# Kernel optimization log

Hardware: AMD Instinct MI355X
Metric: run time of the kernel (lower is better)

## Reference

```python
import jax, jax.numpy as jnp
import numpy as np

B, T, H = 4, 2048, 1024
N, D = 16, 64  # heads, key_dim (= value_dim)
SCALE = 1.0 / float(D) ** 0.5


def setup_inputs() -> dict:
    key = jax.random.key(0)
    ks = jax.random.split(key, 10)
    s = 0.02
    return {
        "query": jax.random.normal(ks[0], (B, T, H), jnp.float32),
        "value": jax.random.normal(ks[1], (B, T, H), jnp.float32),
        "Wq": jax.random.normal(ks[2], (N * D, H), jnp.float32) * s,
        "bq": jnp.zeros((N * D,), jnp.float32),
        "Wk": jax.random.normal(ks[3], (N * D, H), jnp.float32) * s,
        "bk": jnp.zeros((N * D,), jnp.float32),
        "Wv": jax.random.normal(ks[4], (N * D, H), jnp.float32) * s,
        "bv": jnp.zeros((N * D,), jnp.float32),
        "Wo": jax.random.normal(ks[5], (H, N * D), jnp.float32) * s,
        "bo": jnp.zeros((H,), jnp.float32),
    }


def reference(query, value, Wq, bq, Wk, bk, Wv, bv, Wo, bo):
    key_in = value  # key=None path: key = value
    q = (query @ Wq.T + bq).reshape(B, -1, N, D)   # [B,T,N,D]
    k = (key_in @ Wk.T + bk).reshape(B, -1, N, D)  # [B,S,N,D]
    v = (value @ Wv.T + bv).reshape(B, -1, N, D)   # [B,S,N,D]
    # scores [T,S,B,N], softmax over S (axis=1), scaled dot-product
    scores = jnp.einsum('btnd,bsnd->tsbn', q, k) * SCALE
    attn = jax.nn.softmax(scores, axis=1)
    # output [B,T,N,D]
    out = jnp.einsum('tsbn,bsnd->btnd', attn, v)
    out = out.reshape(B, T, N * D)
    return out @ Wo.T + bo
```

## Files before the change

### kernel.cpp

```cpp
#include <hip/hip_runtime.h>
#include <cstdint>
#include <cstddef>

typedef unsigned short u16;
typedef __bf16 bf16x8 __attribute__((ext_vector_type(8)));
typedef __bf16 bf16x2 __attribute__((ext_vector_type(2)));
typedef float f32x4 __attribute__((ext_vector_type(4)));
typedef float f32x16 __attribute__((ext_vector_type(16)));

#define B_   4
#define T_   2048
#define H_   1024
#define NH_  16
#define DH_  64
#define M_   (B_ * T_)
#define KDIM 1024
#define QSCALE 0.18033688011112042f

#define BM 128
#define BN 128
#define BK 32

__device__ __forceinline__ u16 f2bf(float f) {
    unsigned u = __float_as_uint(f);
    unsigned r = (u + 0x7fffu + ((u >> 16) & 1u)) >> 16;
    return (u16)r;
}

__device__ __forceinline__ unsigned packbf2(float a, float b) {
    bf16x2 v = { (__bf16)a, (__bf16)b };
    return __builtin_bit_cast(unsigned, v);
}

__device__ __forceinline__ float exp2_fast(float x) {
#if __has_builtin(__builtin_amdgcn_exp2f)
    return __builtin_amdgcn_exp2f(x);
#else
    return exp2f(x);
#endif
}

__device__ __forceinline__ void plswap(unsigned &a, unsigned &b) {
#if __has_builtin(__builtin_amdgcn_permlane32_swap)
    auto r = __builtin_amdgcn_permlane32_swap(a, b, false, false);
    a = (unsigned)r[0]; b = (unsigned)r[1];
#else
    int hi = (threadIdx.x & 32);
    unsigned x = (unsigned)__shfl_xor((int)(hi ? b : a), 32);
    unsigned na = hi ? x : a;
    unsigned nb = hi ? b : x;
    a = na; b = nb;
#endif
}

__device__ __forceinline__ void gload16(const void* g, void* l) {
    __builtin_amdgcn_global_load_lds(
        (const __attribute__((address_space(1))) unsigned int*)g,
        (__attribute__((address_space(3))) unsigned int*)l,
        16, 0, 0);
}

__device__ __forceinline__ f32x16 mfma32(bf16x8 a, bf16x8 b, f32x16 c) {
    return __builtin_amdgcn_mfma_f32_32x32x16_bf16(a, b, c, 0, 0, 0);
}

__global__ __launch_bounds__(256) void f2bf_hex(
    const float* s0, u16* d0, int n0, const float* s1, u16* d1, int n1,
    const float* s2, u16* d2, int n2, const float* s3, u16* d3, int n3,
    const float* s4, u16* d4, int n4j, const float* s5, u16* d5, int n5)
{
    const float* s; u16* d; int n;
    switch (blockIdx.y) {
        case 0: s = s0; d = d0; n = n0; break;
        case 1: s = s1; d = d1; n = n1; break;
        case 2: s = s2; d = d2; n = n2; break;
        case 3: s = s3; d = d3; n = n3; break;
        case 4: s = s4; d = d4; n = n4j; break;
        default: s = s5; d = d5; n = n5; break;
    }
    int i = blockIdx.x * blockDim.x + threadIdx.x;
    int stride = gridDim.x * blockDim.x;
    for (; i < n; i += stride) {
        float4 f = reinterpret_cast<const float4*>(s)[i];
        ushort4 o;
        o.x = f2bf(f.x); o.y = f2bf(f.y); o.z = f2bf(f.z); o.w = f2bf(f.w);
        reinterpret_cast<ushort4*>(d)[i] = o;
    }
}

__device__ __forceinline__ void gemm_core(
    const u16* __restrict__ X, const u16* __restrict__ W,
    const float* __restrict__ bias,
    u16* __restrict__ dst_bf, float* __restrict__ dst_f,
    float scale, int mode, int r0, int c0)
{
    __shared__ u16 lds[17408];
    char* ldsA = (char*)lds;
    char* ldsB = (char*)lds + 8192;

    const int tid = threadIdx.x;
    const int wid = tid >> 6;
    const int l15 = tid & 15;
    const int l4  = (tid & 63) >> 4;
    const int wr = wid >> 1, wc = wid & 1;

    const u16* gA = X + (size_t)(r0 + (tid >> 2)) * KDIM + (tid & 3) * 8;
    const u16* gB = W + (size_t)(c0 + (tid >> 2)) * KDIM + (tid & 3) * 8;
    char* sA0 = ldsA + wid * 1024;
    char* sA1 = ldsA + 4096 + wid * 1024;
    char* sB0 = ldsB + wid * 1024;
    char* sB1 = ldsB + 4096 + wid * 1024;

    f32x4 acc[4][4];
#pragma unroll
    for (int m = 0; m < 4; ++m)
#pragma unroll
        for (int n = 0; n < 4; ++n) acc[m][n] = (f32x4){0.f, 0.f, 0.f, 0.f};

    gload16(gA, sA0); gload16(gA + 64 * KDIM, sA1);
    gload16(gB, sB0); gload16(gB + 64 * KDIM, sB1);

    const int arow = wr * 64 + l15;
    const int brow = wc * 64 + l15;

    for (int kt = 0; kt < KDIM / BK; ++kt) {
        __syncthreads();
        bf16x8 a[4], b[4];
#pragma unroll
        for (int m = 0; m < 4; ++m)
            a[m] = *(const bf16x8*)(ldsA + (arow + m * 16) * 64 + l4 * 16);
#pragma unroll
        for (int n = 0; n < 4; ++n)
            b[n] = *(const bf16x8*)(ldsB + (brow + n * 16) * 64 + l4 * 16);
#pragma unroll
        for (int m = 0; m < 4; ++m)
#pragma unroll
            for (int n = 0; n < 4; ++n)
                acc[m][n] = __builtin_amdgcn_mfma_f32_16x16x32_bf16(a[m], b[n], acc[m][n], 0, 0, 0);
        __syncthreads();
        if (kt + 1 < KDIM / BK) {
            const u16* pa = gA + (kt + 1) * BK;
            const u16* pb = gB + (kt + 1) * BK;
            gload16(pa, sA0); gload16(pa + 64 * KDIM, sA1);
            gload16(pb, sB0); gload16(pb + 64 * KDIM, sB1);
        }
    }

    if (mode == 2) {
#pragma unroll
        for (int m = 0; m < 4; ++m)
#pragma unroll
            for (int n = 0; n < 4; ++n) {
                int cg = c0 + wc * 64 + n * 16 + l15;
                float bv = bias[cg];
                int rg = r0 + wr * 64 + m * 16 + l4 * 4;
#pragma unroll
                for (int j = 0; j < 4; ++j)
                    dst_f[(size_t)(rg + j) * H_ + cg] = acc[m][n][j] + bv;
            }
    } else if (mode == 0) {
#pragma unroll
        for (int m = 0; m < 4; ++m)
#pragma unroll
            for (int n = 0; n < 4; ++n) {
                int cg = c0 + wc * 64 + n * 16 + l15;
                int head = cg >> 6, d = cg & 63;
                float bv = bias[cg];
                int rg = r0 + wr * 64 + m * 16 + l4 * 4;
#pragma unroll
                for (int j = 0; j < 4; ++j) {
                    int r = rg + j;
                    int b = r >> 11, t = r & (T_ - 1);
                    dst_bf[(((size_t)(b * NH_ + head) * T_ + t) << 6) + d] =
                        f2bf((acc[m][n][j] + bv) * scale);
                }
            }
    } else {
        __syncthreads();
        u16 (*ldsT)[136] = (u16(*)[136])lds;
#pragma unroll
        for (int m = 0; m < 4; ++m)
#pragma unroll
            for (int n = 0; n < 4; ++n) {
                int cl = wc * 64 + n * 16 + l15;
                float bv = bias[c0 + cl];
                int rl = wr * 64 + m * 16 + l4 * 4;
#pragma unroll
                for (int j = 0; j < 4; ++j)
                    ldsT[cl][rl + j] = f2bf(acc[m][n][j] + bv);
            }
        __syncthreads();
        int b = r0 >> 11, tb = r0 & (T_ - 1);
#pragma unroll
        for (int it = 0; it < 8; ++it) {
            int chunk = tid + it * 256;
            int cl = chunk >> 4;
            int r8 = (chunk & 15) << 3;
            int cg = c0 + cl;
            int head = cg >> 6, d = cg & 63;
            uint4 v = *(const uint4*)&ldsT[cl][r8];
            *(uint4*)&dst_bf[((size_t)((b * NH_ + head) * DH_ + d) * T_) + tb + r8] = v;
        }
    }
}

__global__ __launch_bounds__(256) void gemm_qkv(
    const u16* __restrict__ qbf, const u16* __restrict__ vbf,
    const u16* __restrict__ Wqb, const u16* __restrict__ Wkb, const u16* __restrict__ Wvb,
    const float* __restrict__ bq, const float* __restrict__ bk, const float* __restrict__ bv,
    u16* __restrict__ Qd, u16* __restrict__ Kd, u16* __restrict__ Vtd)
{
    const int orig = blockIdx.y * 24 + blockIdx.x;
    const int swz = (orig & 7) * 192 + (orig >> 3);
    const int bx = swz % 24;
    const int by = swz / 24;
    const int seg = bx >> 3;
    const int r0 = by * BM;
    const int c0 = (bx & 7) * BN;

    if (seg == 0)
        gemm_core(qbf, Wqb, bq, Qd, nullptr, QSCALE, 0, r0, c0);
    else if (seg == 1)
        gemm_core(vbf, Wkb, bk, Kd, nullptr, 1.0f, 0, r0, c0);
    else
        gemm_core(vbf, Wvb, bv, Vtd, nullptr, 1.0f, 1, r0, c0);
}

__global__ __launch_bounds__(256) void gemm_out(
    const u16* __restrict__ AO, const u16* __restrict__ Wob,
    const float* __restrict__ bo, float* __restrict__ out)
{
    const int orig = blockIdx.y * 8 + blockIdx.x;
    const int swz = (orig & 7) * 64 + (orig >> 3);
    const int bx = swz & 7;
    const int by = swz >> 3;
    gemm_core(AO, Wob, bo, nullptr, out, 1.0f, 2, by * BM, bx * BN);
}

#define KVB 64

__global__ __launch_bounds__(256) void attn32(
    const u16* __restrict__ Q, const u16* __restrict__ K,
    const u16* __restrict__ Vt, u16* __restrict__ AO)
{
    __shared__ u16 lds[16384];
    char* const base = (char*)lds;

    const int tid = threadIdx.x;
    const int wid = tid >> 6;
    const int lane = tid & 63;
    const int l31 = lane & 31;
    const int hi = lane >> 5;

    const int orig = blockIdx.y * 16 + blockIdx.x;
    const int swz = (orig & 7) * 128 + (orig >> 3);
    const int bn = swz >> 4;
    const int q0 = (swz & 15) * 128 + wid * 32;
    const int b = bn >> 4, head = bn & 15;

    const u16* Qb = Q + ((size_t)bn * T_ + q0 + l31) * DH_;
    const u16* Kb = K + (size_t)bn * T_ * DH_;
    const u16* Vb = Vt + (size_t)bn * DH_ * T_;

    bf16x8 qf[4];
#pragma unroll
    for (int c = 0; c < 4; ++c)
        qf[c] = *(const bf16x8*)(Qb + c * 16 + hi * 8);

    bf16x8 ones;
#pragma unroll
    for (int e = 0; e < 8; ++e) ones[e] = (__bf16)1.0f;

    f32x16 accO0, accO1, Lacc;
#pragma unroll
    for (int r = 0; r < 16; ++r) { accO0[r] = 0.f; accO1[r] = 0.f; Lacc[r] = 0.f; }

    const int srow = tid >> 3;
    const int scsw = (tid & 7) ^ (srow & 7);
    const int rowsw = l31 & 7;

    const u16* kSrc = Kb + (size_t)srow * DH_ + scsw * 8;
    const u16* vSrc = Vb + (size_t)srow * T_ + scsw * 8;

#define STAGE(dK, dV) do { \
    gload16(kSrc,            (dK) + tid * 16); \
    gload16(kSrc + 32 * DH_, (dK) + 4096 + tid * 16); \
    gload16(vSrc,            (dV) + tid * 16); \
    gload16(vSrc + 32 * T_,  (dV) + 4096 + tid * 16); \
    kSrc += KVB * DH_; vSrc += KVB; } while (0)

    char* const kb0 = base;
    char* const vb0 = base + 8192;
    char* const kb1 = base + 16384;
    char* const vb1 = base + 24576;

    auto process = [&](const char* kc, const char* vc) {
        f32x16 sa0, sa1;
#pragma unroll
        for (int r = 0; r < 16; ++r) { sa0[r] = 0.f; sa1[r] = 0.f; }
        __builtin_amdgcn_s_setprio(1);
#pragma unroll
        for (int c = 0; c < 4; ++c) {
            const int c16 = ((2 * c + hi) ^ rowsw) * 16;
            bf16x8 k0 = *(const bf16x8*)(kc + l31 * 128 + c16);
            bf16x8 k1 = *(const bf16x8*)(kc + 4096 + l31 * 128 + c16);
            sa0 = mfma32(k0, qf[c], sa0);
            sa1 = mfma32(k1, qf[c], sa1);
        }
        __builtin_amdgcn_s_setprio(0);

#pragma unroll
        for (int r = 0; r < 16; ++r) {
            sa0[r] = exp2_fast(sa0[r]);
            sa1[r] = exp2_fast(sa1[r]);
        }

        unsigned w0[8], w1[8];
#pragma unroll
        for (int k2 = 0; k2 < 8; ++k2) {
            w0[k2] = packbf2(sa0[2 * k2], sa0[2 * k2 + 1]);
            w1[k2] = packbf2(sa1[2 * k2], sa1[2 * k2 + 1]);
        }
        plswap(w0[0], w0[2]); plswap(w0[1], w0[3]);
        plswap(w0[4], w0[6]); plswap(w0[5], w0[7]);
        plswap(w1[0], w1[2]); plswap(w1[1], w1[3]);
        plswap(w1[4], w1[6]); plswap(w1[5], w1[7]);

        __builtin_amdgcn_s_setprio(1);
#pragma unroll
        for (int ks = 0; ks < 4; ++ks) {
            union { unsigned w[4]; bf16x8 v; } pu;
            const unsigned* src = (ks < 2) ? w0 : w1;
            const int o = (ks & 1) * 4;
            pu.w[0] = src[o + 0]; pu.w[1] = src[o + 1];
            pu.w[2] = src[o + 2]; pu.w[3] = src[o + 3];
            const int c16 = ((2 * ks + hi) ^ rowsw) * 16;
            bf16x8 v0f = *(const bf16x8*)(vc + l31 * 128 + c16);
            bf16x8 v1f = *(const bf16x8*)(vc + 4096 + l31 * 128 + c16);
            accO0 = mfma32(v0f, pu.v, accO0);
            accO1 = mfma32(v1f, pu.v, accO1);
            Lacc  = mfma32(ones, pu.v, Lacc);
        }
        __builtin_amdgcn_s_setprio(0);
    };

    STAGE(kb0, vb0);
    __syncthreads();

    for (int it = 0; it < T_ / KVB; it += 2) {
        STAGE(kb1, vb1);
        process(kb0, vb0);
        __syncthreads();
        if (it + 2 < T_ / KVB) STAGE(kb0, vb0);
        process(kb1, vb1);
        __syncthreads();
    }

    char* myO = base + wid * 4096;
    float inv = 1.f / Lacc[0];
#pragma unroll
    for (int n = 0; n < 2; ++n)
#pragma unroll
        for (int r = 0; r < 16; ++r) {
            int d = n * 32 + (r & 3) + 8 * (r >> 2) + 4 * hi;
            int c16 = (d >> 3) ^ rowsw;
            float v = (n == 0 ? accO0[r] : accO1[r]) * inv;
            *(u16*)(myO + l31 * 128 + c16 * 16 + (d & 7) * 2) = f2bf(v);
        }
    asm volatile("s_waitcnt lgkmcnt(0)" ::: "memory");
#pragma unroll
    for (int it = 0; it < 4; ++it) {
        int id = lane + it * 64;
        int row = id >> 3, c = id & 7;
        int c16s = c ^ (row & 7);
        uint4 val = *(const uint4*)(myO + row * 128 + c16s * 16);
        *(uint4*)&AO[(size_t)(b * T_ + q0 + row) * (NH_ * DH_) + head * DH_ + c * 8] = val;
    }
#undef STAGE
}

extern "C" void kernel_launch(void* const* d_in, const int* in_sizes, int n_in,
                              void* d_out, int out_size, void* d_ws, size_t ws_size,
                              hipStream_t stream)
{
    const float* query = (const float*)d_in[0];
    const float* value = (const float*)d_in[1];
    const float* Wq = (const float*)d_in[2];
    const float* bq = (const float*)d_in[3];
    const float* Wk = (const float*)d_in[4];
    const float* bk = (const float*)d_in[5];
    const float* Wv = (const float*)d_in[6];
    const float* bv = (const float*)d_in[7];
    const float* Wo = (const float*)d_in[8];
    const float* bo = (const float*)d_in[9];
    float* out = (float*)d_out;

    u16* ws = (u16*)d_ws;
    const size_t E8M = (size_t)8 << 20;
    u16* qbf = ws;
    u16* vbf = ws + E8M;
    u16* Wqb = ws + 2 * E8M;
    u16* Wkb = Wqb + (1u << 20);
    u16* Wvb = Wkb + (1u << 20);
    u16* Wob = Wvb + (1u << 20);
    u16* Qd  = Wob + (1u << 20);
    u16* Kd  = Qd + E8M;
    u16* Vtd = Kd + E8M;
    u16* AO  = Vtd + E8M;

    const int nBig = (B_ * T_ * H_) / 4;
    const int nW   = (KDIM * KDIM) / 4;
    f2bf_hex<<<dim3(512, 6), 256, 0, stream>>>(
        query, qbf, nBig, value, vbf, nBig,
        Wq, Wqb, nW, Wk, Wkb, nW, Wv, Wvb, nW, Wo, Wob, nW);

    gemm_qkv<<<dim3(24, 64), 256, 0, stream>>>(qbf, vbf, Wqb, Wkb, Wvb,
                                               bq, bk, bv, Qd, Kd, Vtd);

    attn32<<<dim3(16, 64), 256, 0, stream>>>(Qd, Kd, Vtd, AO);

    gemm_out<<<dim3(8, 64), 256, 0, stream>>>(AO, Wob, bo, out);
}
```

Before: 209.6 us.

## Double per-wave query rows in attention and stage Q/K stores through LDS

After: 196.8 us. 1.06x faster.

```diff
diff --git a/kernel.cpp b/kernel.cpp
--- a/kernel.cpp
+++ b/kernel.cpp
@@ -159,22 +159,31 @@
                     dst_f[(size_t)(rg + j) * H_ + cg] = acc[m][n][j] + bv;
             }
     } else if (mode == 0) {
+        __syncthreads();
+        u16 (*ldsR)[136] = (u16(*)[136])lds;
 #pragma unroll
         for (int m = 0; m < 4; ++m)
 #pragma unroll
             for (int n = 0; n < 4; ++n) {
-                int cg = c0 + wc * 64 + n * 16 + l15;
-                int head = cg >> 6, d = cg & 63;
-                float bv = bias[cg];
-                int rg = r0 + wr * 64 + m * 16 + l4 * 4;
-#pragma unroll
-                for (int j = 0; j < 4; ++j) {
-                    int r = rg + j;
-                    int b = r >> 11, t = r & (T_ - 1);
-                    dst_bf[(((size_t)(b * NH_ + head) * T_ + t) << 6) + d] =
-                        f2bf((acc[m][n][j] + bv) * scale);
-                }
+                int cl = wc * 64 + n * 16 + l15;
+                float bv = bias[c0 + cl];
+                int rl = wr * 64 + m * 16 + l4 * 4;
+#pragma unroll
+                for (int j = 0; j < 4; ++j)
+                    ldsR[rl + j][cl] = f2bf((acc[m][n][j] + bv) * scale);
             }
+        __syncthreads();
+        int b2 = r0 >> 11, tb = r0 & (T_ - 1);
+#pragma unroll
+        for (int it = 0; it < 8; ++it) {
+            int id = tid + it * 256;
+            int row = id >> 4;
+            int ch = id & 15;
+            int head = (c0 >> 6) + (ch >> 3);
+            int d0 = (ch & 7) * 8;
+            uint4 v = *(const uint4*)&ldsR[row][ch * 8];
+            *(uint4*)&dst_bf[(((size_t)(b2 * NH_ + head) * T_ + tb + row) << 6) + d0] = v;
+        }
     } else {
         __syncthreads();
         u16 (*ldsT)[136] = (u16(*)[136])lds;
@@ -239,7 +248,7 @@
 
 #define KVB 64
 
-__global__ __launch_bounds__(256) void attn32(
+__global__ __launch_bounds__(256, 2) void attn64(
     const u16* __restrict__ Q, const u16* __restrict__ K,
     const u16* __restrict__ Vt, u16* __restrict__ AO)
 {
@@ -252,28 +261,34 @@
     const int l31 = lane & 31;
     const int hi = lane >> 5;
 
-    const int orig = blockIdx.y * 16 + blockIdx.x;
-    const int swz = (orig & 7) * 128 + (orig >> 3);
-    const int bn = swz >> 4;
-    const int q0 = (swz & 15) * 128 + wid * 32;
+    const int orig = blockIdx.y * 8 + blockIdx.x;
+    const int swz = (orig & 7) * 64 + (orig >> 3);
+    const int bn = swz >> 3;
+    const int q0w = (swz & 7) * 256 + wid * 64;
     const int b = bn >> 4, head = bn & 15;
 
-    const u16* Qb = Q + ((size_t)bn * T_ + q0 + l31) * DH_;
+    const u16* Qb = Q + ((size_t)bn * T_ + q0w + l31) * DH_;
     const u16* Kb = K + (size_t)bn * T_ * DH_;
     const u16* Vb = Vt + (size_t)bn * DH_ * T_;
 
-    bf16x8 qf[4];
-#pragma unroll
-    for (int c = 0; c < 4; ++c)
-        qf[c] = *(const bf16x8*)(Qb + c * 16 + hi * 8);
+    bf16x8 qfa[4], qfb[4];
+#pragma unroll
+    for (int c = 0; c < 4; ++c) {
+        qfa[c] = *(const bf16x8*)(Qb + c * 16 + hi * 8);
+        qfb[c] = *(const bf16x8*)(Qb + 32 * DH_ + c * 16 + hi * 8);
+    }
 
     bf16x8 ones;
 #pragma unroll
     for (int e = 0; e < 8; ++e) ones[e] = (__bf16)1.0f;
 
-    f32x16 accO0, accO1, Lacc;
-#pragma unroll
-    for (int r = 0; r < 16; ++r) { accO0[r] = 0.f; accO1[r] = 0.f; Lacc[r] = 0.f; }
+    f32x16 accO00, accO01, accO10, accO11, La, Lb;
+#pragma unroll
+    for (int r = 0; r < 16; ++r) {
+        accO00[r] = 0.f; accO01[r] = 0.f;
+        accO10[r] = 0.f; accO11[r] = 0.f;
+        La[r] = 0.f; Lb[r] = 0.f;
+    }
 
     const int srow = tid >> 3;
     const int scsw = (tid & 7) ^ (srow & 7);
@@ -295,51 +310,67 @@
     char* const vb1 = base + 24576;
 
     auto process = [&](const char* kc, const char* vc) {
-        f32x16 sa0, sa1;
-#pragma unroll
-        for (int r = 0; r < 16; ++r) { sa0[r] = 0.f; sa1[r] = 0.f; }
+        f32x16 sA0, sA1, sB0, sB1;
+#pragma unroll
+        for (int r = 0; r < 16; ++r) { sA0[r] = 0.f; sA1[r] = 0.f; sB0[r] = 0.f; sB1[r] = 0.f; }
         __builtin_amdgcn_s_setprio(1);
 #pragma unroll
         for (int c = 0; c < 4; ++c) {
             const int c16 = ((2 * c + hi) ^ rowsw) * 16;
             bf16x8 k0 = *(const bf16x8*)(kc + l31 * 128 + c16);
             bf16x8 k1 = *(const bf16x8*)(kc + 4096 + l31 * 128 + c16);
-            sa0 = mfma32(k0, qf[c], sa0);
-            sa1 = mfma32(k1, qf[c], sa1);
+            sA0 = mfma32(k0, qfa[c], sA0);
+            sA1 = mfma32(k1, qfa[c], sA1);
+            sB0 = mfma32(k0, qfb[c], sB0);
+            sB1 = mfma32(k1, qfb[c], sB1);
         }
         __builtin_amdgcn_s_setprio(0);
 
 #pragma unroll
         for (int r = 0; r < 16; ++r) {
-            sa0[r] = exp2_fast(sa0[r]);
-            sa1[r] = exp2_fast(sa1[r]);
-        }
-
-        unsigned w0[8], w1[8];
+            sA0[r] = exp2_fast(sA0[r]);
+            sA1[r] = exp2_fast(sA1[r]);
+            sB0[r] = exp2_fast(sB0[r]);
+            sB1[r] = exp2_fast(sB1[r]);
+        }
+
+        unsigned w0a[8], w1a[8], w0b[8], w1b[8];
 #pragma unroll
         for (int k2 = 0; k2 < 8; ++k2) {
-            w0[k2] = packbf2(sa0[2 * k2], sa0[2 * k2 + 1]);
-            w1[k2] = packbf2(sa1[2 * k2], sa1[2 * k2 + 1]);
-        }
-        plswap(w0[0], w0[2]); plswap(w0[1], w0[3]);
-        plswap(w0[4], w0[6]); plswap(w0[5], w0[7]);
-        plswap(w1[0], w1[2]); plswap(w1[1], w1[3]);
-        plswap(w1[4], w1[6]); plswap(w1[5], w1[7]);
+            w0a[k2] = packbf2(sA0[2 * k2], sA0[2 * k2 + 1]);
+            w1a[k2] = packbf2(sA1[2 * k2], sA1[2 * k2 + 1]);
+            w0b[k2] = packbf2(sB0[2 * k2], sB0[2 * k2 + 1]);
+            w1b[k2] = packbf2(sB1[2 * k2], sB1[2 * k2 + 1]);
+        }
+        plswap(w0a[0], w0a[2]); plswap(w0a[1], w0a[3]);
+        plswap(w0a[4], w0a[6]); plswap(w0a[5], w0a[7]);
+        plswap(w1a[0], w1a[2]); plswap(w1a[1], w1a[3]);
+        plswap(w1a[4], w1a[6]); plswap(w1a[5], w1a[7]);
+        plswap(w0b[0], w0b[2]); plswap(w0b[1], w0b[3]);
+        plswap(w0b[4], w0b[6]); plswap(w0b[5], w0b[7]);
+        plswap(w1b[0], w1b[2]); plswap(w1b[1], w1b[3]);
+        plswap(w1b[4], w1b[6]); plswap(w1b[5], w1b[7]);
 
         __builtin_amdgcn_s_setprio(1);
 #pragma unroll
         for (int ks = 0; ks < 4; ++ks) {
-            union { unsigned w[4]; bf16x8 v; } pu;
-            const unsigned* src = (ks < 2) ? w0 : w1;
+            union { unsigned w[4]; bf16x8 v; } pa, pb;
+            const unsigned* sa_ = (ks < 2) ? w0a : w1a;
+            const unsigned* sb_ = (ks < 2) ? w0b : w1b;
             const int o = (ks & 1) * 4;
-            pu.w[0] = src[o + 0]; pu.w[1] = src[o + 1];
-            pu.w[2] = src[o + 2]; pu.w[3] = src[o + 3];
+            pa.w[0] = sa_[o + 0]; pa.w[1] = sa_[o + 1];
+            pa.w[2] = sa_[o + 2]; pa.w[3] = sa_[o + 3];
+            pb.w[0] = sb_[o + 0]; pb.w[1] = sb_[o + 1];
+            pb.w[2] = sb_[o + 2]; pb.w[3] = sb_[o + 3];
             const int c16 = ((2 * ks + hi) ^ rowsw) * 16;
             bf16x8 v0f = *(const bf16x8*)(vc + l31 * 128 + c16);
             bf16x8 v1f = *(const bf16x8*)(vc + 4096 + l31 * 128 + c16);
-            accO0 = mfma32(v0f, pu.v, accO0);
-            accO1 = mfma32(v1f, pu.v, accO1);
-            Lacc  = mfma32(ones, pu.v, Lacc);
+            accO00 = mfma32(v0f, pa.v, accO00);
+            accO01 = mfma32(v1f, pa.v, accO01);
+            accO10 = mfma32(v0f, pb.v, accO10);
+            accO11 = mfma32(v1f, pb.v, accO11);
+            La = mfma32(ones, pa.v, La);
+            Lb = mfma32(ones, pb.v, Lb);
         }
         __builtin_amdgcn_s_setprio(0);
     };
@@ -356,25 +387,29 @@
         __syncthreads();
     }
 
-    char* myO = base + wid * 4096;
-    float inv = 1.f / Lacc[0];
+    char* myO = base + wid * 8192;
+    float inva = 1.f / La[0];
+    float invb = 1.f / Lb[0];
 #pragma unroll
     for (int n = 0; n < 2; ++n)
 #pragma unroll
         for (int r = 0; r < 16; ++r) {
             int d = n * 32 + (r & 3) + 8 * (r >> 2) + 4 * hi;
             int c16 = (d >> 3) ^ rowsw;
-            float v = (n == 0 ? accO0[r] : accO1[r]) * inv;
-            *(u16*)(myO + l31 * 128 + c16 * 16 + (d & 7) * 2) = f2bf(v);
+            float va = (n == 0 ? accO00[r] : accO01[r]) * inva;
+            float vb2 = (n == 0 ? accO10[r] : accO11[r]) * invb;
+            *(u16*)(myO + l31 * 128 + c16 * 16 + (d & 7) * 2) = f2bf(va);
+            *(u16*)(myO + (32 + l31) * 128 + c16 * 16 + (d & 7) * 2) = f2bf(vb2);
         }
     asm volatile("s_waitcnt lgkmcnt(0)" ::: "memory");
 #pragma unroll
-    for (int it = 0; it < 4; ++it) {
+    for (int it = 0; it < 8; ++it) {
         int id = lane + it * 64;
-        int row = id >> 3, c = id & 7;
+        int row = id >> 3;
+        int c = id & 7;
         int c16s = c ^ (row & 7);
         uint4 val = *(const uint4*)(myO + row * 128 + c16s * 16);
-        *(uint4*)&AO[(size_t)(b * T_ + q0 + row) * (NH_ * DH_) + head * DH_ + c * 8] = val;
+        *(uint4*)&AO[(size_t)(b * T_ + q0w + row) * (NH_ * DH_) + head * DH_ + c * 8] = val;
     }
 #undef STAGE
 }
@@ -417,7 +452,7 @@
     gemm_qkv<<<dim3(24, 64), 256, 0, stream>>>(qbf, vbf, Wqb, Wkb, Wvb,
                                                bq, bk, bv, Qd, Kd, Vtd);
 
-    attn32<<<dim3(16, 64), 256, 0, stream>>>(Qd, Kd, Vtd, AO);
+    attn64<<<dim3(8, 64), 256, 0, stream>>>(Qd, Kd, Vtd, AO);
 
     gemm_out<<<dim3(8, 64), 256, 0, stream>>>(AO, Wob, bo, out);
 }
```
